# Kernel optimization log

Measured on AMD Instinct MI355X. Metric: run time of the kernel, lower is better.

The kernel has to match this reference:

```python
import jax, jax.numpy as jnp
import numpy as np

B, L, HID = 1, 2048, 4096
H, KV, D = 32, 2, 128
ROT = int(D * 0.5)  # partial rotary dims per head
THETA = 10000.0
SCALE = D ** -0.5


def _rope_tables(L, rot, theta):
    inv_freq = 1.0 / (theta ** (np.arange(0, rot, 2, dtype=np.float32) / rot))  # [rot/2]
    t = np.arange(L, dtype=np.float32)
    freqs = np.outer(t, inv_freq)  # [L, rot/2]
    return jnp.asarray(np.cos(freqs)), jnp.asarray(np.sin(freqs))


def setup_inputs() -> dict:
    key = jax.random.key(0)
    ks = jax.random.split(key, 8)
    s = HID ** -0.5
    x = jax.random.normal(ks[0], (B, L, HID), dtype=jnp.float32)
    Wq = jax.random.normal(ks[1], (HID, H * D), dtype=jnp.float32) * s
    Wk = jax.random.normal(ks[2], (HID, KV * D), dtype=jnp.float32) * s
    Wv = jax.random.normal(ks[3], (HID, KV * D), dtype=jnp.float32) * s
    Wo = jax.random.normal(ks[4], (H * D, HID), dtype=jnp.float32) * s
    bq = jax.random.normal(ks[5], (H * D,), dtype=jnp.float32) * 0.01
    bk = jax.random.normal(ks[6], (KV * D,), dtype=jnp.float32) * 0.01
    bv = jax.random.normal(ks[7], (KV * D,), dtype=jnp.float32) * 0.01
    cos, sin = _rope_tables(L, ROT, THETA)
    # additive causal mask
    causal = jnp.tril(jnp.ones((L, L), dtype=bool))
    attention_mask = jnp.where(causal, 0.0, -1e9)[None, None].astype(jnp.float32)
    return {"x": x, "Wq": Wq, "bq": bq, "Wk": Wk, "bk": bk, "Wv": Wv, "bv": bv,
            "Wo": Wo, "cos": cos, "sin": sin, "attention_mask": attention_mask}


def _apply_rope(t, cos, sin):
    # t: [B, h, L, D]; rotary on first ROT dims, pass-through on the rest
    t_rot, t_pass = t[..., :ROT], t[..., ROT:]
    x1, x2 = t_rot[..., : ROT // 2], t_rot[..., ROT // 2:]
    c = cos[None, None]  # [1,1,L,ROT/2]
    s = sin[None, None]
    rot = jnp.concatenate([x1 * c - x2 * s, x2 * c + x1 * s], axis=-1)
    return jnp.concatenate([rot, t_pass], axis=-1)


def reference(x, Wq, bq, Wk, bk, Wv, bv, Wo, cos, sin, attention_mask):
    Bx, Lx, _ = x.shape
    q = (x @ Wq + bq).reshape(Bx, Lx, H, D).transpose(0, 2, 1, 3)   # [B,H,L,D]
    k = (x @ Wk + bk).reshape(Bx, Lx, KV, D).transpose(0, 2, 1, 3)  # [B,KV,L,D]
    v = (x @ Wv + bv).reshape(Bx, Lx, KV, D).transpose(0, 2, 1, 3)
    q = _apply_rope(q, cos, sin)
    k = _apply_rope(k, cos, sin)
    # GQA: repeat KV heads
    rep = H // KV
    k = jnp.repeat(k, rep, axis=1)  # [B,H,L,D]
    v = jnp.repeat(v, rep, axis=1)
    w = jnp.einsum('bhqd,bhkd->bhqk', q, k) * SCALE + attention_mask
    w = jax.nn.softmax(w, axis=-1)
    o = jnp.einsum('bhqk,bhkd->bhqd', w, v)
    o = o.transpose(0, 2, 1, 3).reshape(Bx, Lx, H * D)
    return o @ Wo
```

## Files before the change

kernel.cpp:

```cpp
#include <hip/hip_runtime.h>
#include <stdint.h>

#define L_SEQ 2048
#define HID   4096
#define NH    32
#define NKV   2
#define DH    128
#define NQKV  4608
#define QSCALE 0.088388347648318447f

typedef __bf16 bf16x8 __attribute__((ext_vector_type(8)));
typedef float  f32x4  __attribute__((ext_vector_type(4)));

__device__ __forceinline__ unsigned short f2bf(float f) {
  union { float f; unsigned u; } cv; cv.f = f;
  unsigned u = cv.u;
  return (unsigned short)((u + 0x7fffu + ((u >> 16) & 1u)) >> 16);
}
__device__ __forceinline__ float bf2f(unsigned short h) {
  union { unsigned u; float f; } cv; cv.u = (unsigned)h << 16; return cv.f;
}
__device__ __forceinline__ unsigned pk2(float a, float b) {
  return (unsigned)f2bf(a) | ((unsigned)f2bf(b) << 16);
}

#define GLL16(gsrc, ldst)                                                              \
  __builtin_amdgcn_global_load_lds(                                                    \
      (const __attribute__((address_space(1))) unsigned int*)(gsrc),                   \
      (__attribute__((address_space(3))) unsigned int*)(ldst), 16, 0, 0)

__global__ __launch_bounds__(256) void cast_bf16_kernel(const float* __restrict__ in,
                                                        unsigned short* __restrict__ out,
                                                        int n4) {
  int i = blockIdx.x * 256 + threadIdx.x;
  if (i >= n4) return;
  float4 v = reinterpret_cast<const float4*>(in)[i];
  ushort4 o;
  o.x = f2bf(v.x); o.y = f2bf(v.y); o.z = f2bf(v.z); o.w = f2bf(v.w);
  reinterpret_cast<ushort4*>(out)[i] = o;
}

__global__ __launch_bounds__(256) void transpose_cast_kernel(const float* __restrict__ in,
                                                             unsigned short* __restrict__ out,
                                                             int R, int C) {
  __shared__ float tile[64][65];
  const int c0 = blockIdx.x * 64, r0 = blockIdx.y * 64;
  const int tid = threadIdx.x;
  #pragma unroll
  for (int it = 0; it < 4; ++it) {
    int row = it * 16 + (tid >> 4);
    float4 v = *reinterpret_cast<const float4*>(&in[(size_t)(r0 + row) * C + c0 + (tid & 15) * 4]);
    tile[row][(tid & 15) * 4 + 0] = v.x;
    tile[row][(tid & 15) * 4 + 1] = v.y;
    tile[row][(tid & 15) * 4 + 2] = v.z;
    tile[row][(tid & 15) * 4 + 3] = v.w;
  }
  __syncthreads();
  #pragma unroll
  for (int it = 0; it < 8; ++it) {
    int c  = it * 8 + (tid >> 5);
    int rp = tid & 31;
    unsigned u = (unsigned)f2bf(tile[2 * rp][c]) | ((unsigned)f2bf(tile[2 * rp + 1][c]) << 16);
    *reinterpret_cast<unsigned*>(&out[(size_t)(c0 + c) * R + r0 + 2 * rp]) = u;
  }
}

__global__ __launch_bounds__(256) void vtrans_kernel(const unsigned short* __restrict__ in,
                                                     unsigned short* __restrict__ out) {
  __shared__ unsigned short tile[64][72];
  const int l0 = blockIdx.x * 64, d0 = blockIdx.y * 64, g = blockIdx.z;
  const int tid = threadIdx.x;
  #pragma unroll
  for (int it = 0; it < 2; ++it) {
    int l = it * 32 + (tid >> 3);
    *reinterpret_cast<uint4*>(&tile[l][(tid & 7) * 8]) =
        *reinterpret_cast<const uint4*>(&in[((size_t)g * L_SEQ + l0 + l) * DH + d0 + (tid & 7) * 8]);
  }
  __syncthreads();
  #pragma unroll
  for (int it = 0; it < 2; ++it) {
    int d = it * 32 + (tid >> 3);
    unsigned short tmp[8];
    #pragma unroll
    for (int e = 0; e < 8; ++e) tmp[e] = tile[(tid & 7) * 8 + e][d];
    *reinterpret_cast<uint4*>(&out[((size_t)g * DH + d0 + d) * L_SEQ + l0 + (tid & 7) * 8]) =
        *reinterpret_cast<uint4*>(tmp);
  }
}

#define TBM 128
#define TBN 128
#define TBK 32

template <int MODE>
__global__ __launch_bounds__(256, 4) void gemm128_kernel(const unsigned short* __restrict__ A,
                                                         const unsigned short* __restrict__ Bt,
                                                         float* __restrict__ C,
                                                         const float* __restrict__ bq,
                                                         const float* __restrict__ bk,
                                                         const float* __restrict__ bv,
                                                         const float* __restrict__ cosT,
                                                         const float* __restrict__ sinT,
                                                         unsigned short* __restrict__ qb,
                                                         unsigned short* __restrict__ kb,
                                                         unsigned short* __restrict__ vlin,
                                                         int M, int N, int K) {
  __shared__ __attribute__((aligned(16))) unsigned short As[2][TBM * TBK];
  __shared__ __attribute__((aligned(16))) unsigned short Bs[2][TBN * TBK];
  const int tid = threadIdx.x;
  const int wave = tid >> 6, lane = tid & 63;
  const int lg = lane >> 4, ll = lane & 15;
  const int wm = wave >> 1, wn = wave & 1;

  int gx = gridDim.x, nwg = gx * gridDim.y;
  int flat = blockIdx.y * gx + blockIdx.x;
  int bx = blockIdx.x, by = blockIdx.y;
  if ((nwg & 7) == 0) {
    int t = (flat & 7) * (nwg >> 3) + (flat >> 3);
    bx = t % gx; by = t / gx;
  }
  const int m0 = by * TBM, n0 = bx * TBN;

  f32x4 acc[4][4] = {};
  const int NT = K >> 5;

  auto stage = [&](int t, int buf) {
    const int k0 = t * TBK;
    #pragma unroll
    for (int i = 0; i < 2; ++i) {
      int ci  = (i * 4 + wave) * 64 + lane;
      int row = ci >> 2;
      int cg  = (ci & 3) ^ ((row >> 1) & 3);
      GLL16(A + (size_t)(m0 + row) * K + k0 + cg * 8, &As[buf][(i * 4 + wave) * 512]);
    }
    #pragma unroll
    for (int i = 0; i < 2; ++i) {
      int ci  = (i * 4 + wave) * 64 + lane;
      int row = ci >> 2;
      int cg  = (ci & 3) ^ ((row >> 1) & 3);
      GLL16(Bt + (size_t)(n0 + row) * K + k0 + cg * 8, &Bs[buf][(i * 4 + wave) * 512]);
    }
  };

  stage(0, 0);
  stage(1, 1);

  for (int t = 0; t < NT; ++t) {
    const int cur = t & 1;
    if (t + 1 < NT) asm volatile("s_waitcnt vmcnt(4)" ::: "memory");
    else            asm volatile("s_waitcnt vmcnt(0)" ::: "memory");
    __builtin_amdgcn_s_barrier();

    const unsigned short* Ac = &As[cur][0];
    const unsigned short* Bc = &Bs[cur][0];
    bf16x8 afr[4], bfr[4];
    #pragma unroll
    for (int i = 0; i < 4; ++i) {
      int ra = wm * 64 + i * 16 + ll;
      afr[i] = *reinterpret_cast<const bf16x8*>(
          &Ac[ra * 32 + ((lg ^ ((ra >> 1) & 3)) * 8)]);
      int rb = wn * 64 + i * 16 + ll;
      bfr[i] = *reinterpret_cast<const bf16x8*>(
          &Bc[rb * 32 + ((lg ^ ((rb >> 1) & 3)) * 8)]);
    }
    asm volatile("s_waitcnt lgkmcnt(0)" ::: "memory");
    __builtin_amdgcn_s_barrier();
    if (t + 2 < NT) stage(t + 2, cur);

    __builtin_amdgcn_s_setprio(1);
    #pragma unroll
    for (int i = 0; i < 4; ++i)
      #pragma unroll
      for (int j = 0; j < 4; ++j)
        acc[i][j] = __builtin_amdgcn_mfma_f32_16x16x32_bf16(afr[i], bfr[j], acc[i][j], 0, 0, 0);
    __builtin_amdgcn_s_setprio(0);
  }

  if (MODE == 0) {
    #pragma unroll
    for (int i = 0; i < 4; ++i)
      #pragma unroll
      for (int j = 0; j < 4; ++j) {
        int col  = n0 + wn * 64 + j * 16 + ll;
        int rowb = m0 + wm * 64 + i * 16 + lg * 4;
        #pragma unroll
        for (int r = 0; r < 4; ++r)
          C[(size_t)(rowb + r) * N + col] = acc[i][j][r];
      }
  } else {
    const int region = (n0 < 4096) ? 0 : ((n0 < 4352) ? 1 : 2);
    const int hh = (region == 0) ? (n0 >> 7) : ((region == 1) ? ((n0 - 4096) >> 7) : ((n0 - 4352) >> 7));
    const float* bias = (region == 0) ? bq : ((region == 1) ? bk : bv);
    #pragma unroll
    for (int j = 0; j < 4; ++j) {
      float bj = bias[hh * DH + wn * 64 + j * 16 + ll];
      #pragma unroll
      for (int i = 0; i < 4; ++i)
        #pragma unroll
        for (int r = 0; r < 4; ++r) acc[i][j][r] += bj;
    }
    if (region < 2 && wn == 0) {
      #pragma unroll
      for (int i = 0; i < 4; ++i)
        #pragma unroll
        for (int r = 0; r < 4; ++r) {
          int l = m0 + wm * 64 + i * 16 + lg * 4 + r;
          float c0 = cosT[l * 32 + ll],      s0 = sinT[l * 32 + ll];
          float c1 = cosT[l * 32 + 16 + ll], s1 = sinT[l * 32 + 16 + ll];
          float x10 = acc[i][0][r], x20 = acc[i][2][r];
          float x11 = acc[i][1][r], x21 = acc[i][3][r];
          acc[i][0][r] = x10 * c0 - x20 * s0;
          acc[i][2][r] = x20 * c0 + x10 * s0;
          acc[i][1][r] = x11 * c1 - x21 * s1;
          acc[i][3][r] = x21 * c1 + x11 * s1;
        }
    }
    const float scale = (region == 0) ? QSCALE : 1.f;
    unsigned short* dst = (region == 0) ? qb : ((region == 1) ? kb : vlin);
    #pragma unroll
    for (int i = 0; i < 4; ++i)
      #pragma unroll
      for (int j = 0; j < 4; ++j) {
        int d = wn * 64 + j * 16 + ll;
        #pragma unroll
        for (int r = 0; r < 4; ++r) {
          int l = m0 + wm * 64 + i * 16 + lg * 4 + r;
          dst[((size_t)hh * L_SEQ + l) * DH + d] = f2bf(acc[i][j][r] * scale);
        }
      }
  }
}

__global__ __launch_bounds__(256, 2) void attn_kernel(const unsigned short* __restrict__ qg,
                                                      const unsigned short* __restrict__ kb,
                                                      const unsigned short* __restrict__ vt,
                                                      unsigned short* __restrict__ ob) {
  __shared__ __attribute__((aligned(16))) unsigned short Ks[2][64 * 128];
  __shared__ __attribute__((aligned(16))) unsigned short Vs[2][128 * 64];

  const int pair = blockIdx.x, h = blockIdx.y;
  const int g = h >> 4;
  const int tid = threadIdx.x, wave = tid >> 6, lane = tid & 63;
  const int lg = lane >> 4, ll = lane & 15;

  const int krow = (lane >> 4);
  const int kcg0 = (lane & 15);
  const int vrow = (lane >> 3);
  const int vcg0 = (lane & 7);

  #pragma unroll
  for (int seg = 0; seg < 2; ++seg) {
    const int qt = seg ? (31 - pair) : pair;
    const int q0 = qt * 64 + wave * 16;

    bf16x8 qf[4];
    #pragma unroll
    for (int f = 0; f < 4; ++f)
      qf[f] = *reinterpret_cast<const bf16x8*>(
          qg + ((size_t)h * L_SEQ + q0 + ll) * DH + f * 32 + lg * 8);

    f32x4 of[8] = {};
    float m = -1e30f, lsum = 0.f;

    const int kvN = qt + 1;
    int cur = 0;

    #pragma unroll
    for (int c = 0; c < 4; ++c) {
      int issue = wave * 4 + c;
      int rk = issue * 4 + krow;
      GLL16(kb + ((size_t)g * L_SEQ + rk) * DH + (kcg0 ^ (rk & 7)) * 8, &Ks[0][issue * 512]);
      int rv = issue * 8 + vrow;
      GLL16(vt + ((size_t)g * DH + rv) * L_SEQ + (vcg0 ^ (rv & 7)) * 8, &Vs[0][issue * 512]);
    }
    __syncthreads();

    for (int t = 0; t < kvN; ++t) {
      if (t + 1 < kvN) {
        int kv1 = (t + 1) * 64;
        #pragma unroll
        for (int c = 0; c < 4; ++c) {
          int issue = wave * 4 + c;
          int rk = issue * 4 + krow;
          GLL16(kb + ((size_t)g * L_SEQ + kv1 + rk) * DH + (kcg0 ^ (rk & 7)) * 8,
                &Ks[cur ^ 1][issue * 512]);
          int rv = issue * 8 + vrow;
          GLL16(vt + ((size_t)g * DH + rv) * L_SEQ + kv1 + (vcg0 ^ (rv & 7)) * 8,
                &Vs[cur ^ 1][issue * 512]);
        }
      }

      f32x4 s[4] = {};
      const unsigned short* Kc = &Ks[cur][0];
      #pragma unroll
      for (int cf = 0; cf < 4; ++cf) {
        bf16x8 kf[4];
        #pragma unroll
        for (int f = 0; f < 4; ++f) {
          int rk = cf * 16 + ll;
          int cc = (f * 4 + lg) ^ (rk & 7);
          kf[f] = *reinterpret_cast<const bf16x8*>(&Kc[rk * 128 + cc * 8]);
        }
        __builtin_amdgcn_s_setprio(1);
        #pragma unroll
        for (int f = 0; f < 4; ++f)
          s[cf] = __builtin_amdgcn_mfma_f32_16x16x32_bf16(kf[f], qf[f], s[cf], 0, 0, 0);
        __builtin_amdgcn_s_setprio(0);
      }

      if (t == qt) {
        #pragma unroll
        for (int cf = 0; cf < 4; ++cf)
          #pragma unroll
          for (int r = 0; r < 4; ++r)
            if (cf * 16 + lg * 4 + r > wave * 16 + ll) s[cf][r] = -1e30f;
      }

      float pmax = -1e30f;
      #pragma unroll
      for (int cf = 0; cf < 4; ++cf)
        #pragma unroll
        for (int r = 0; r < 4; ++r) pmax = fmaxf(pmax, s[cf][r]);
      if (!__all(pmax - m <= 8.f)) {
        float mx = fmaxf(pmax, __shfl_xor(pmax, 16));
        mx = fmaxf(mx, __shfl_xor(mx, 32));
        float mnew = fmaxf(m, mx);
        float alpha = __expf(m - mnew);
        m = mnew;
        lsum *= alpha;
        float af[4];
        #pragma unroll
        for (int r = 0; r < 4; ++r) af[r] = __shfl(alpha, lg * 4 + r);
        #pragma unroll
        for (int ds = 0; ds < 8; ++ds)
          #pragma unroll
          for (int r = 0; r < 4; ++r) of[ds][r] *= af[r];
      }

      unsigned wlo[4], whi[4];
      float psum = 0.f;
      #pragma unroll
      for (int cf = 0; cf < 4; ++cf) {
        float p0 = __expf(s[cf][0] - m), p1 = __expf(s[cf][1] - m);
        float p2 = __expf(s[cf][2] - m), p3 = __expf(s[cf][3] - m);
        psum += (p0 + p1) + (p2 + p3);
        wlo[cf] = pk2(p0, p1);
        whi[cf] = pk2(p2, p3);
      }
      lsum += psum;

      bf16x8 pa[2];
      {
        const int src0 = ((lg & 1) << 5) + ll;
        const int src1 = src0 + 16;
        const bool hi = (lg & 2) != 0;
        #pragma unroll
        for (int ks = 0; ks < 2; ++ks) {
          int e0a = __shfl((int)wlo[ks * 2], src0);
          int e1a = __shfl((int)whi[ks * 2], src0);
          int e2a = __shfl((int)wlo[ks * 2], src1);
          int e3a = __shfl((int)whi[ks * 2], src1);
          int e0b = __shfl((int)wlo[ks * 2 + 1], src0);
          int e1b = __shfl((int)whi[ks * 2 + 1], src0);
          int e2b = __shfl((int)wlo[ks * 2 + 1], src1);
          int e3b = __shfl((int)whi[ks * 2 + 1], src1);
          union { int i[4]; bf16x8 v; } u;
          u.i[0] = hi ? e0b : e0a;
          u.i[1] = hi ? e1b : e1a;
          u.i[2] = hi ? e2b : e2a;
          u.i[3] = hi ? e3b : e3a;
          pa[ks] = u.v;
        }
      }

      const unsigned short* Vc = &Vs[cur][0];
      #pragma unroll
      for (int ds = 0; ds < 8; ++ds) {
        bf16x8 vf[2];
        #pragma unroll
        for (int ks = 0; ks < 2; ++ks) {
          int dl = ds * 16 + ll;
          int cc = (ks * 4 + lg) ^ (dl & 7);
          vf[ks] = *reinterpret_cast<const bf16x8*>(&Vc[dl * 64 + cc * 8]);
        }
        __builtin_amdgcn_s_setprio(1);
        #pragma unroll
        for (int ks = 0; ks < 2; ++ks)
          of[ds] = __builtin_amdgcn_mfma_f32_16x16x32_bf16(pa[ks], vf[ks], of[ds], 0, 0, 0);
        __builtin_amdgcn_s_setprio(0);
      }

      __syncthreads();
      cur ^= 1;
    }

    float tot = lsum + __shfl_xor(lsum, 16);
    tot += __shfl_xor(tot, 32);
    float inv = 1.f / tot;
    float invr[4];
    #pragma unroll
    for (int r = 0; r < 4; ++r) invr[r] = __shfl(inv, lg * 4 + r);
    #pragma unroll
    for (int ds = 0; ds < 8; ++ds)
      #pragma unroll
      for (int r = 0; r < 4; ++r) {
        int row = q0 + lg * 4 + r;
        ob[(size_t)row * (NH * DH) + h * DH + ds * 16 + ll] = f2bf(of[ds][r] * invr[r]);
      }
    __syncthreads();
  }
}

extern "C" void kernel_launch(void* const* d_in, const int* in_sizes, int n_in,
                              void* d_out, int out_size, void* d_ws, size_t ws_size,
                              hipStream_t stream) {
  (void)in_sizes; (void)n_in; (void)out_size; (void)ws_size;
  const float* x    = (const float*)d_in[0];
  const float* Wq   = (const float*)d_in[1];
  const float* bq   = (const float*)d_in[2];
  const float* Wk   = (const float*)d_in[3];
  const float* bk   = (const float*)d_in[4];
  const float* Wv   = (const float*)d_in[5];
  const float* bv   = (const float*)d_in[6];
  const float* Wo   = (const float*)d_in[7];
  const float* cosT = (const float*)d_in[8];
  const float* sinT = (const float*)d_in[9];

  char* ws = (char*)d_ws;
  size_t off = 0;
  auto alloc = [&](size_t bytes) { void* p = ws + off; off += (bytes + 255) & ~(size_t)255; return p; };
  unsigned short* xb    = (unsigned short*)alloc((size_t)L_SEQ * HID * 2);
  unsigned short* Wqkvt = (unsigned short*)alloc((size_t)NQKV * HID * 2);
  unsigned short* Wot   = (unsigned short*)alloc((size_t)HID * HID * 2);
  unsigned short* qbuf  = (unsigned short*)alloc((size_t)NH * L_SEQ * DH * 2);
  unsigned short* kbuf  = (unsigned short*)alloc((size_t)NKV * L_SEQ * DH * 2);
  unsigned short* vlin  = (unsigned short*)alloc((size_t)NKV * L_SEQ * DH * 2);
  unsigned short* vtb   = (unsigned short*)alloc((size_t)NKV * DH * L_SEQ * 2);
  unsigned short* attno = (unsigned short*)alloc((size_t)L_SEQ * HID * 2);

  cast_bf16_kernel<<<(L_SEQ * HID / 4 + 255) / 256, 256, 0, stream>>>(x, xb, L_SEQ * HID / 4);
  transpose_cast_kernel<<<dim3(HID / 64, HID / 64), 256, 0, stream>>>(Wq, Wqkvt, HID, HID);
  transpose_cast_kernel<<<dim3(256 / 64, HID / 64), 256, 0, stream>>>(Wk, Wqkvt + (size_t)4096 * HID, HID, 256);
  transpose_cast_kernel<<<dim3(256 / 64, HID / 64), 256, 0, stream>>>(Wv, Wqkvt + (size_t)4352 * HID, HID, 256);
  transpose_cast_kernel<<<dim3(HID / 64, HID / 64), 256, 0, stream>>>(Wo, Wot, HID, HID);

  gemm128_kernel<1><<<dim3(NQKV / TBN, L_SEQ / TBM), 256, 0, stream>>>(
      xb, Wqkvt, nullptr, bq, bk, bv, cosT, sinT, qbuf, kbuf, vlin, L_SEQ, NQKV, HID);

  vtrans_kernel<<<dim3(L_SEQ / 64, DH / 64, NKV), 256, 0, stream>>>(vlin, vtb);

  attn_kernel<<<dim3(16, NH), 256, 0, stream>>>(qbuf, kbuf, vtb, attno);

  gemm128_kernel<0><<<dim3(HID / TBN, L_SEQ / TBM), 256, 0, stream>>>(
      attno, Wot, (float*)d_out, nullptr, nullptr, nullptr, nullptr, nullptr,
      nullptr, nullptr, nullptr, L_SEQ, HID, HID);
}
```

Measured before the change: 319.9 us.

## Fuse weight preprocessing launches and overlap Wo transpose with QKV GEMM

Merges the x cast and the Wq/Wk/Wv transpose-casts into a single preprocessing kernel. It also appends the Wo transpose-cast as extra blocks in the QKV GEMM launch, using a 1D grid with flat block indexing. This removes several kernel launches and inter-kernel gaps, and lets the memory-bound Wo conversion overlap with the compute-bound GEMM tail. Extra transpose blocks in the GEMM launch may compete with GEMM blocks for CU resources and bandwidth.

```diff
diff --git a/kernel.cpp b/kernel.cpp
--- a/kernel.cpp
+++ b/kernel.cpp
@@ -29,39 +29,57 @@
       (const __attribute__((address_space(1))) unsigned int*)(gsrc),                   \
       (__attribute__((address_space(3))) unsigned int*)(ldst), 16, 0, 0)
 
-__global__ __launch_bounds__(256) void cast_bf16_kernel(const float* __restrict__ in,
-                                                        unsigned short* __restrict__ out,
-                                                        int n4) {
-  int i = blockIdx.x * 256 + threadIdx.x;
-  if (i >= n4) return;
-  float4 v = reinterpret_cast<const float4*>(in)[i];
-  ushort4 o;
-  o.x = f2bf(v.x); o.y = f2bf(v.y); o.z = f2bf(v.z); o.w = f2bf(v.w);
-  reinterpret_cast<ushort4*>(out)[i] = o;
-}
-
-__global__ __launch_bounds__(256) void transpose_cast_kernel(const float* __restrict__ in,
-                                                             unsigned short* __restrict__ out,
-                                                             int R, int C) {
-  __shared__ float tile[64][65];
-  const int c0 = blockIdx.x * 64, r0 = blockIdx.y * 64;
-  const int tid = threadIdx.x;
+__device__ __forceinline__ void transpose_tile(const float* __restrict__ in,
+                                               unsigned short* __restrict__ out,
+                                               int R, int C, int bx, int by,
+                                               float* tile , int tid) {
+  const int c0 = bx * 64, r0 = by * 64;
   #pragma unroll
   for (int it = 0; it < 4; ++it) {
     int row = it * 16 + (tid >> 4);
     float4 v = *reinterpret_cast<const float4*>(&in[(size_t)(r0 + row) * C + c0 + (tid & 15) * 4]);
-    tile[row][(tid & 15) * 4 + 0] = v.x;
-    tile[row][(tid & 15) * 4 + 1] = v.y;
-    tile[row][(tid & 15) * 4 + 2] = v.z;
-    tile[row][(tid & 15) * 4 + 3] = v.w;
+    tile[row * 65 + (tid & 15) * 4 + 0] = v.x;
+    tile[row * 65 + (tid & 15) * 4 + 1] = v.y;
+    tile[row * 65 + (tid & 15) * 4 + 2] = v.z;
+    tile[row * 65 + (tid & 15) * 4 + 3] = v.w;
   }
   __syncthreads();
   #pragma unroll
   for (int it = 0; it < 8; ++it) {
     int c  = it * 8 + (tid >> 5);
     int rp = tid & 31;
-    unsigned u = (unsigned)f2bf(tile[2 * rp][c]) | ((unsigned)f2bf(tile[2 * rp + 1][c]) << 16);
+    unsigned u = (unsigned)f2bf(tile[2 * rp * 65 + c]) |
+                 ((unsigned)f2bf(tile[(2 * rp + 1) * 65 + c]) << 16);
     *reinterpret_cast<unsigned*>(&out[(size_t)(c0 + c) * R + r0 + 2 * rp]) = u;
+  }
+}
+
+__global__ __launch_bounds__(256) void preproc_kernel(const float* __restrict__ x,
+                                                      unsigned short* __restrict__ xb,
+                                                      const float* __restrict__ Wq,
+                                                      const float* __restrict__ Wk,
+                                                      const float* __restrict__ Wv,
+                                                      unsigned short* __restrict__ Wqkvt) {
+  __shared__ __attribute__((aligned(16))) float tile[64 * 65];
+  const int tid = threadIdx.x;
+  int bid = blockIdx.x;
+  if (bid < 8192) {
+    int i = bid * 256 + tid;
+    float4 v = reinterpret_cast<const float4*>(x)[i];
+    ushort4 o;
+    o.x = f2bf(v.x); o.y = f2bf(v.y); o.z = f2bf(v.z); o.w = f2bf(v.w);
+    reinterpret_cast<ushort4*>(xb)[i] = o;
+    return;
+  }
+  bid -= 8192;
+  if (bid < 4096) {
+    transpose_tile(Wq, Wqkvt, HID, HID, bid & 63, bid >> 6, tile, tid);
+  } else if (bid < 4352) {
+    bid -= 4096;
+    transpose_tile(Wk, Wqkvt + (size_t)4096 * HID, HID, 256, bid & 3, bid >> 2, tile, tid);
+  } else {
+    bid -= 4352;
+    transpose_tile(Wv, Wqkvt + (size_t)4352 * HID, HID, 256, bid & 3, bid >> 2, tile, tid);
   }
 }
 
@@ -104,19 +122,31 @@
                                                          unsigned short* __restrict__ qb,
                                                          unsigned short* __restrict__ kb,
                                                          unsigned short* __restrict__ vlin,
+                                                         const float* __restrict__ Wo,
+                                                         unsigned short* __restrict__ Wot,
                                                          int M, int N, int K) {
-  __shared__ __attribute__((aligned(16))) unsigned short As[2][TBM * TBK];
-  __shared__ __attribute__((aligned(16))) unsigned short Bs[2][TBN * TBK];
+  __shared__ __attribute__((aligned(16))) unsigned short smem[2 * TBM * TBK + 2 * TBN * TBK];
   const int tid = threadIdx.x;
+  const int gx = N >> 7;
+  const int nwgg = (M >> 7) * gx;
+  const int flat = blockIdx.x;
+
+  if (MODE == 1 && flat >= nwgg) {
+    int tb = flat - nwgg;
+    transpose_tile(Wo, Wot, HID, HID, tb & 63, tb >> 6,
+                   reinterpret_cast<float*>(smem), tid);
+    return;
+  }
+
+  unsigned short* Asb = smem;
+  unsigned short* Bsb = smem + 2 * TBM * TBK;
   const int wave = tid >> 6, lane = tid & 63;
   const int lg = lane >> 4, ll = lane & 15;
   const int wm = wave >> 1, wn = wave & 1;
 
-  int gx = gridDim.x, nwg = gx * gridDim.y;
-  int flat = blockIdx.y * gx + blockIdx.x;
-  int bx = blockIdx.x, by = blockIdx.y;
-  if ((nwg & 7) == 0) {
-    int t = (flat & 7) * (nwg >> 3) + (flat >> 3);
+  int bx = flat % gx, by = flat / gx;
+  if ((nwgg & 7) == 0) {
+    int t = (flat & 7) * (nwgg >> 3) + (flat >> 3);
     bx = t % gx; by = t / gx;
   }
   const int m0 = by * TBM, n0 = bx * TBN;
@@ -131,14 +161,14 @@
       int ci  = (i * 4 + wave) * 64 + lane;
       int row = ci >> 2;
       int cg  = (ci & 3) ^ ((row >> 1) & 3);
-      GLL16(A + (size_t)(m0 + row) * K + k0 + cg * 8, &As[buf][(i * 4 + wave) * 512]);
+      GLL16(A + (size_t)(m0 + row) * K + k0 + cg * 8, &Asb[buf * TBM * TBK + (i * 4 + wave) * 512]);
     }
     #pragma unroll
     for (int i = 0; i < 2; ++i) {
       int ci  = (i * 4 + wave) * 64 + lane;
       int row = ci >> 2;
       int cg  = (ci & 3) ^ ((row >> 1) & 3);
-      GLL16(Bt + (size_t)(n0 + row) * K + k0 + cg * 8, &Bs[buf][(i * 4 + wave) * 512]);
+      GLL16(Bt + (size_t)(n0 + row) * K + k0 + cg * 8, &Bsb[buf * TBN * TBK + (i * 4 + wave) * 512]);
     }
   };
 
@@ -151,8 +181,8 @@
     else            asm volatile("s_waitcnt vmcnt(0)" ::: "memory");
     __builtin_amdgcn_s_barrier();
 
-    const unsigned short* Ac = &As[cur][0];
-    const unsigned short* Bc = &Bs[cur][0];
+    const unsigned short* Ac = &Asb[cur * TBM * TBK];
+    const unsigned short* Bc = &Bsb[cur * TBN * TBK];
     bf16x8 afr[4], bfr[4];
     #pragma unroll
     for (int i = 0; i < 4; ++i) {
@@ -438,20 +468,17 @@
   unsigned short* vtb   = (unsigned short*)alloc((size_t)NKV * DH * L_SEQ * 2);
   unsigned short* attno = (unsigned short*)alloc((size_t)L_SEQ * HID * 2);
 
-  cast_bf16_kernel<<<(L_SEQ * HID / 4 + 255) / 256, 256, 0, stream>>>(x, xb, L_SEQ * HID / 4);
-  transpose_cast_kernel<<<dim3(HID / 64, HID / 64), 256, 0, stream>>>(Wq, Wqkvt, HID, HID);
-  transpose_cast_kernel<<<dim3(256 / 64, HID / 64), 256, 0, stream>>>(Wk, Wqkvt + (size_t)4096 * HID, HID, 256);
-  transpose_cast_kernel<<<dim3(256 / 64, HID / 64), 256, 0, stream>>>(Wv, Wqkvt + (size_t)4352 * HID, HID, 256);
-  transpose_cast_kernel<<<dim3(HID / 64, HID / 64), 256, 0, stream>>>(Wo, Wot, HID, HID);
-
-  gemm128_kernel<1><<<dim3(NQKV / TBN, L_SEQ / TBM), 256, 0, stream>>>(
-      xb, Wqkvt, nullptr, bq, bk, bv, cosT, sinT, qbuf, kbuf, vlin, L_SEQ, NQKV, HID);
+  preproc_kernel<<<12800, 256, 0, stream>>>(x, xb, Wq, Wk, Wv, Wqkvt);
+
+  gemm128_kernel<1><<<576 + 4096, 256, 0, stream>>>(
+      xb, Wqkvt, nullptr, bq, bk, bv, cosT, sinT, qbuf, kbuf, vlin,
+      Wo, Wot, L_SEQ, NQKV, HID);
 
   vtrans_kernel<<<dim3(L_SEQ / 64, DH / 64, NKV), 256, 0, stream>>>(vlin, vtb);
 
   attn_kernel<<<dim3(16, NH), 256, 0, stream>>>(qbuf, kbuf, vtb, attno);
 
-  gemm128_kernel<0><<<dim3(HID / TBN, L_SEQ / TBM), 256, 0, stream>>>(
+  gemm128_kernel<0><<<512, 256, 0, stream>>>(
       attno, Wot, (float*)d_out, nullptr, nullptr, nullptr, nullptr, nullptr,
-      nullptr, nullptr, nullptr, L_SEQ, HID, HID);
-}
+      nullptr, nullptr, nullptr, nullptr, nullptr, L_SEQ, HID, HID);
+}
```

Measured after the change: 330.2 us. +3.2%, slower.
